# Kernel tuning notes

Hardware: AMD Instinct MI355X
Metric: run time of the kernel (lower is better)

The kernel has to match this reference:

```python
import jax, jax.numpy as jnp
import numpy as np

# Static problem sizes
B, C, T, H, W = 2, 256, 16, 64, 64
N = 128                      # number of ROIs
OT, OH, OW = 2, 7, 7         # output_size (t, h, w)
SS, TS = 1.0, 1.0            # spatial_scale, temporal_scale
T_EXT_MAX, S_EXT_MAX = 16, 32  # max ROI extents (by construction of rois)
# adaptive_max_pool bin length is bounded by ceil(L/O)+1
KT = (T_EXT_MAX + OT - 1) // OT + 1   # 9
KS = (S_EXT_MAX + OH - 1) // OH + 1   # 6


def setup_inputs() -> dict:
    key = jax.random.key(0)
    features = jax.random.normal(key, (B, C, T, H, W), dtype=jnp.float32)
    rng = np.random.default_rng(0)
    bidx = rng.integers(0, B, N)
    te = rng.integers(4, T_EXT_MAX + 1, N)
    t1 = rng.integers(0, T - te + 1)
    t2 = t1 + te - 1
    he = rng.integers(8, S_EXT_MAX + 1, N)
    y1 = rng.integers(0, H - he + 1)
    y2 = y1 + he - 1
    we = rng.integers(8, S_EXT_MAX + 1, N)
    x1 = rng.integers(0, W - we + 1)
    x2 = x1 + we - 1
    # layout: (batch_idx, t1, x1, y1, t2, x2, y2)
    rois = np.stack([bidx, t1, x1, y1, t2, x2, y2], axis=1).astype(np.float32)
    return {"features": features, "rois": jnp.asarray(rois)}


def _bin_idx(start, length, O, K):
    """Adaptive-pool bin indices for one dim. Returns abs indices [O,K] and validity mask."""
    o = jnp.arange(O)
    s = (o * length) // O                      # floor(o*L/O)
    e = ((o + 1) * length + O - 1) // O        # ceil((o+1)*L/O)
    idx = s[:, None] + jnp.arange(K)[None, :]  # [O, K]
    valid = idx < e[:, None]
    return start + jnp.minimum(idx, length - 1), valid


def _pool_one(roi, features):
    b = roi[0].astype(jnp.int32)
    # source scales coords cols [1,2,3,4] by spatial_scale and [0,5] by temporal_scale
    scale = jnp.array([TS, SS, SS, SS, SS, TS], dtype=roi.dtype)
    c = jnp.floor(roi[1:7] * scale).astype(jnp.int32)
    t1, x1, y1, t2, x2, y2 = c[0], c[1], c[2], c[3], c[4], c[5]
    feat = features[b]  # [C, T, H, W]
    neg = -jnp.inf
    # W dimension
    wi, wv = _bin_idx(x1, x2 - x1 + 1, OW, KS)
    x = feat[:, :, :, wi]                                    # [C,T,H,OW,KS]
    x = jnp.where(wv, x, neg).max(axis=-1)                   # [C,T,H,OW]
    # H dimension
    hi, hv = _bin_idx(y1, y2 - y1 + 1, OH, KS)
    x = jnp.take(x, hi.reshape(-1), axis=2).reshape(C, T, OH, KS, OW)
    x = jnp.where(hv[None, None, :, :, None], x, neg).max(axis=3)  # [C,T,OH,OW]
    # T dimension
    ti, tv = _bin_idx(t1, t2 - t1 + 1, OT, KT)
    x = jnp.take(x, ti.reshape(-1), axis=1).reshape(C, OT, KT, OH, OW)
    return jnp.where(tv[None, :, :, None, None], x, neg).max(axis=2)  # [C,OT,OH,OW]


def reference(features, rois):
    # sequential map over ROIs keeps peak memory bounded (each ROI pool is fully vectorized)
    return jax.lax.map(lambda r: _pool_one(r, features), rois)  # [N,C,OT,OH,OW]
```

## Files before the change

kernel.cpp:

```cpp
#include <hip/hip_runtime.h>
#include <hip/hip_fp16.h>
#include <math.h>

#define BB 2
#define CC 256
#define TT 16
#define HH 64
#define WW 64
#define NN 128
#define OT 2
#define OH 7
#define OW 7
#define PP (TT * HH * WW)
#define BIN (OT * OH * OW)
#define CU2 (CC / 2)
#define NQ (NN * OH * OW)
#define GRIDP (NQ / 2)

typedef _Float16 hf2 __attribute__((ext_vector_type(2)));

__global__ __launch_bounds__(256) void transpose_f16_kernel(
    const float* __restrict__ in, unsigned int* __restrict__ outt )
{
    __shared__ float tile[64][65];
    int pb = blockIdx.x & 1023;
    int cb = (blockIdx.x >> 10) & 3;
    int b  = blockIdx.x >> 12;

    int tx = threadIdx.x & 63;
    int wv = threadIdx.x >> 6;
    const float* src = in + ((size_t)b * CC + cb * 64) * PP + pb * 64;
    #pragma unroll
    for (int r = 0; r < 16; ++r) {
        int c = wv + r * 4;
        tile[tx][c] = src[(size_t)c * PP + tx];
    }
    __syncthreads();

    int cp   = threadIdx.x & 31;
    int prow = threadIdx.x >> 5;
    size_t base = ((size_t)b * PP + (size_t)pb * 64) * CC + cb * 64;
    #pragma unroll
    for (int r = 0; r < 8; ++r) {
        int p = prow + r * 8;
        __half h0 = __float2half(tile[p][2 * cp]);
        __half h1 = __float2half(tile[p][2 * cp + 1]);
        unsigned int u = (unsigned int)__half_as_ushort(h0)
                       | ((unsigned int)__half_as_ushort(h1) << 16);
        outt[(base + (size_t)p * CC) / 2 + cp] = u;
    }
}

template<int NX, int D>
__device__ __forceinline__ void pool_loop(
    const unsigned int* __restrict__ p, int niter, int ny,
    int ystep, int tstep, hf2& m0, hf2& m1, hf2& m2, hf2& m3)
{
    uint4 v[D][NX];
    int iy = 0;

#define PLOAD(d)                                            \
    _Pragma("unroll")                                       \
    for (int j = 0; j < NX; ++j)                            \
        v[d][j] = *(const uint4*)(p + j * CU2);

#define PADV()                                              \
    do { if (++iy == ny) { iy = 0; p += tstep; } else p += ystep; } while (0)

#define PCONS(d)                                            \
    _Pragma("unroll")                                       \
    for (int j = 0; j < NX; ++j) {                          \
        m0 = __builtin_elementwise_max(m0, __builtin_bit_cast(hf2, v[d][j].x)); \
        m1 = __builtin_elementwise_max(m1, __builtin_bit_cast(hf2, v[d][j].y)); \
        m2 = __builtin_elementwise_max(m2, __builtin_bit_cast(hf2, v[d][j].z)); \
        m3 = __builtin_elementwise_max(m3, __builtin_bit_cast(hf2, v[d][j].w)); \
    }

    if (niter > D) {
        #pragma unroll
        for (int d = 0; d < D; ++d) { PLOAD(d); PADV(); }
        int M = (niter - D) / D;
        int r = (niter - D) % D;
        for (int s = 0; s < M; ++s) {
            #pragma unroll
            for (int d = 0; d < D; ++d) { PCONS(d); PLOAD(d); PADV(); }
        }
        #pragma unroll
        for (int d = 0; d < D - 1; ++d)
            if (d < r) { PCONS(d); PLOAD(d); PADV(); }
        #pragma unroll
        for (int d = 0; d < D; ++d) PCONS(d);
    } else {
        for (int i = 0; i < niter; ++i) { PLOAD(0); PADV(); PCONS(0); }
    }
#undef PLOAD
#undef PADV
#undef PCONS
}

__global__ __launch_bounds__(256) void roipool3d_f16_kernel(
    const unsigned int* __restrict__ featt,
    const float* __restrict__ rois,
    float* __restrict__ out)
{
    __shared__ unsigned int comb[2][64][4];

    int wg  = blockIdx.x;
    int swz = (wg & 7) * (GRIDP / 8) + (wg >> 3);
    int wave  = threadIdx.x >> 6;
    int qslot = wave >> 1;
    int tc    = wave & 1;
    int lane = threadIdx.x & 63;
    int half = lane >> 5;
    int cl   = lane & 31;
    int q    = swz * 2 + qslot;
    int rem  = q % (OH * OW);
    int n    = q / (OH * OW);
    int oh   = rem / OW;
    int ow   = rem % OW;

    const float* r = rois + n * 7;
    int b  = (int)r[0];
    int t1 = (int)r[1];
    int x1 = (int)r[2];
    int y1 = (int)r[3];
    int t2 = (int)r[4];
    int x2 = (int)r[5];
    int y2 = (int)r[6];
    int lt = t2 - t1 + 1, lh = y2 - y1 + 1, lw = x2 - x1 + 1;

    int nt_full = (lt + 1) >> 1;
    int ntc0 = (nt_full + 1) >> 1;
    int nt_c = tc ? (nt_full - ntc0) : ntc0;
    int t0 = t1 + (half ? (lt >> 1) : 0) + (tc ? ntc0 : 0);

    int hs = (oh * lh) / OH, he = ((oh + 1) * lh + OH - 1) / OH;
    int ws = (ow * lw) / OW, we = ((ow + 1) * lw + OW - 1) / OW;
    int ny = he - hs;
    int nx = we - ws;
    int niter = nt_c * ny;

    const unsigned int* p = featt
        + (size_t)((size_t)b * PP + (size_t)((t0 * HH + (y1 + hs)) * WW + (x1 + ws))) * CU2
        + cl * 4;

    const int ystep = WW * CU2;
    const int tstep = (HH - (ny - 1)) * WW * CU2;

    hf2 m0; m0[0] = (_Float16)(-65504.0f); m0[1] = m0[0];
    hf2 m1 = m0, m2 = m0, m3 = m0;

    switch (nx) {
        case 2:  pool_loop<2, 6>(p, niter, ny, ystep, tstep, m0, m1, m2, m3); break;
        case 3:  pool_loop<3, 4>(p, niter, ny, ystep, tstep, m0, m1, m2, m3); break;
        case 4:  pool_loop<4, 3>(p, niter, ny, ystep, tstep, m0, m1, m2, m3); break;
        case 5:  pool_loop<5, 2>(p, niter, ny, ystep, tstep, m0, m1, m2, m3); break;
        default: pool_loop<6, 2>(p, niter, ny, ystep, tstep, m0, m1, m2, m3); break;
    }

    if (tc) {
        comb[qslot][lane][0] = __builtin_bit_cast(unsigned int, m0);
        comb[qslot][lane][1] = __builtin_bit_cast(unsigned int, m1);
        comb[qslot][lane][2] = __builtin_bit_cast(unsigned int, m2);
        comb[qslot][lane][3] = __builtin_bit_cast(unsigned int, m3);
    }
    __syncthreads();
    if (!tc) {
        m0 = __builtin_elementwise_max(m0, __builtin_bit_cast(hf2, comb[qslot][lane][0]));
        m1 = __builtin_elementwise_max(m1, __builtin_bit_cast(hf2, comb[qslot][lane][1]));
        m2 = __builtin_elementwise_max(m2, __builtin_bit_cast(hf2, comb[qslot][lane][2]));
        m3 = __builtin_elementwise_max(m3, __builtin_bit_cast(hf2, comb[qslot][lane][3]));

        int c0 = cl * 8;
        int bin = half * (OH * OW) + rem;
        size_t ob = (size_t)(n * CC + c0) * BIN + bin;
        out[ob]           = (float)m0[0];
        out[ob + BIN]     = (float)m0[1];
        out[ob + 2 * BIN] = (float)m1[0];
        out[ob + 3 * BIN] = (float)m1[1];
        out[ob + 4 * BIN] = (float)m2[0];
        out[ob + 5 * BIN] = (float)m2[1];
        out[ob + 6 * BIN] = (float)m3[0];
        out[ob + 7 * BIN] = (float)m3[1];
    }
}

#define NXCD 8
#define C_PER_XCD (CC / NXCD)
#define PLANE (NN * BIN)
#define BLOCKS_PER_C (PLANE / 256)
__global__ __launch_bounds__(256) void roipool3d_fb_kernel(
    const float* __restrict__ feat, const float* __restrict__ rois,
    float* __restrict__ out)
{
    int wg = blockIdx.x, xcd = wg % NXCD, i = wg / NXCD;
    int c = xcd * C_PER_XCD + i / BLOCKS_PER_C;
    int p = (i % BLOCKS_PER_C) * 256 + threadIdx.x;
    int n = p / BIN, rem = p % BIN;
    int ot = rem / (OH * OW), oh = (rem / OW) % OH, ow = rem % OW;
    const float* r = rois + n * 7;
    int b = (int)r[0], t1 = (int)r[1], x1 = (int)r[2], y1 = (int)r[3];
    int t2 = (int)r[4], x2 = (int)r[5], y2 = (int)r[6];
    int lt = t2 - t1 + 1, lh = y2 - y1 + 1, lw = x2 - x1 + 1;
    int ts = (ot * lt) / OT, te = ((ot + 1) * lt + OT - 1) / OT;
    int hs = (oh * lh) / OH, he = ((oh + 1) * lh + OH - 1) / OH;
    int ws = (ow * lw) / OW, we = ((ow + 1) * lw + OW - 1) / OW;
    const float* fbase = feat + ((size_t)b * CC + c) * PP;
    float m = -INFINITY;
    for (int t = t1 + ts; t < t1 + te; ++t)
        for (int y = y1 + hs; y < y1 + he; ++y)
            for (int x = x1 + ws; x < x1 + we; ++x)
                m = fmaxf(m, fbase[t * (HH * WW) + y * WW + x]);
    out[((size_t)n * CC + c) * BIN + rem] = m;
}

extern "C" void kernel_launch(void* const* d_in, const int* in_sizes, int n_in,
                              void* d_out, int out_size, void* d_ws, size_t ws_size,
                              hipStream_t stream) {
    const float* feat = (const float*)d_in[0];
    const float* rois = (const float*)d_in[1];
    float* out = (float*)d_out;

    size_t need = (size_t)BB * CC * PP * sizeof(unsigned short);
    if (ws_size >= need && d_ws) {
        unsigned int* featt = (unsigned int*)d_ws;
        transpose_f16_kernel<<<BB * 4 * 1024, 256, 0, stream>>>(feat, featt);
        roipool3d_f16_kernel<<<GRIDP, 256, 0, stream>>>(featt, rois, out);
    } else {
        roipool3d_fb_kernel<<<NXCD * C_PER_XCD * BLOCKS_PER_C, 256, 0, stream>>>(
            feat, rois, out);
    }
}
```

Before: 84.11 us.

## Sort ROIs by Morton key and stage channel-contiguous output before untransposing

Adds a single-block bitonic sort that orders ROIs by batch index and a Morton code of their center, so neighbouring workgroups pool spatially nearby regions and share cache lines in the transposed feature buffer. The pooling kernel now writes vectorized channel-contiguous float4 results into a staging buffer instead of eight scattered strided stores. A new untranspose kernel then rewrites the staging buffer into the required [N,C,OT,OH,OW] layout through shared memory. This adds two kernel launches and an extra pass over the output in exchange for better cache locality and coalesced writes.

After: 83.54 us, median of 2. Within noise of the previous version (-0.7%).

```diff
diff --git a/kernel.cpp b/kernel.cpp
--- a/kernel.cpp
+++ b/kernel.cpp
@@ -17,6 +17,12 @@
 #define NQ (NN * OH * OW)
 #define GRIDP (NQ / 2)
 
+#define FEATT_BYTES ((size_t)BB * CC * PP * 2)
+#define STAGE_OFF   FEATT_BYTES
+#define STAGE_BYTES ((size_t)NN * BIN * CC * 4)
+#define PERM_OFF    (STAGE_OFF + ((STAGE_BYTES + 255) & ~(size_t)255))
+#define WS_NEED     (PERM_OFF + NN * 4)
+
 typedef _Float16 hf2 __attribute__((ext_vector_type(2)));
 
 __global__ __launch_bounds__(256) void transpose_f16_kernel(
@@ -49,6 +55,42 @@
                        | ((unsigned int)__half_as_ushort(h1) << 16);
         outt[(base + (size_t)p * CC) / 2 + cp] = u;
     }
+}
+
+__global__ __launch_bounds__(128) void sort_rois_kernel(
+    const float* __restrict__ rois, int* __restrict__ perm)
+{
+    __shared__ unsigned int k[NN];
+    int t = threadIdx.x;
+    const float* r = rois + t * 7;
+    int b  = (int)r[0];
+    int t1 = (int)r[1], x1 = (int)r[2], y1 = (int)r[3];
+    int t2 = (int)r[4], x2 = (int)r[5], y2 = (int)r[6];
+    int tc = (t1 + t2) >> 1;
+    int yc = ((y1 + y2) >> 1) >> 2;
+    int xc = ((x1 + x2) >> 1) >> 2;
+    unsigned int m = 0;
+    #pragma unroll
+    for (int i = 0; i < 4; ++i) {
+        m |= (((unsigned)(tc >> i) & 1u) << (3 * i + 2));
+        m |= (((unsigned)(yc >> i) & 1u) << (3 * i + 1));
+        m |= (((unsigned)(xc >> i) & 1u) << (3 * i));
+    }
+    unsigned int key = ((unsigned)b << 12) | m;
+    k[t] = (key << 8) | (unsigned)t;
+    __syncthreads();
+    for (int kk = 2; kk <= NN; kk <<= 1) {
+        for (int j = kk >> 1; j > 0; j >>= 1) {
+            int ixj = t ^ j;
+            if (ixj > t) {
+                bool up = ((t & kk) == 0);
+                unsigned int a = k[t], c = k[ixj];
+                if ((a > c) == up) { k[t] = c; k[ixj] = a; }
+            }
+            __syncthreads();
+        }
+    }
+    perm[t] = (int)(k[t] & 0xFFu);
 }
 
 template<int NX, int D>
@@ -101,7 +143,8 @@
 __global__ __launch_bounds__(256) void roipool3d_f16_kernel(
     const unsigned int* __restrict__ featt,
     const float* __restrict__ rois,
-    float* __restrict__ out)
+    const int* __restrict__ perm,
+    float* __restrict__ stage)
 {
     __shared__ unsigned int comb[2][64][4];
 
@@ -115,7 +158,7 @@
     int cl   = lane & 31;
     int q    = swz * 2 + qslot;
     int rem  = q % (OH * OW);
-    int n    = q / (OH * OW);
+    int n    = perm[q / (OH * OW)];
     int oh   = rem / OW;
     int ow   = rem % OW;
 
@@ -173,15 +216,30 @@
 
         int c0 = cl * 8;
         int bin = half * (OH * OW) + rem;
-        size_t ob = (size_t)(n * CC + c0) * BIN + bin;
-        out[ob]           = (float)m0[0];
-        out[ob + BIN]     = (float)m0[1];
-        out[ob + 2 * BIN] = (float)m1[0];
-        out[ob + 3 * BIN] = (float)m1[1];
-        out[ob + 4 * BIN] = (float)m2[0];
-        out[ob + 5 * BIN] = (float)m2[1];
-        out[ob + 6 * BIN] = (float)m3[0];
-        out[ob + 7 * BIN] = (float)m3[1];
+        float4 s0 = { (float)m0[0], (float)m0[1], (float)m1[0], (float)m1[1] };
+        float4 s1 = { (float)m2[0], (float)m2[1], (float)m3[0], (float)m3[1] };
+        float* sp = stage + ((size_t)n * BIN + bin) * CC + c0;
+        *(float4*)sp       = s0;
+        *(float4*)(sp + 4) = s1;
+    }
+}
+
+__global__ __launch_bounds__(128) void untranspose_kernel(
+    const float* __restrict__ stage, float* __restrict__ out)
+{
+    __shared__ float t[32][99];
+    int n  = blockIdx.x >> 3;
+    int c0 = (blockIdx.x & 7) * 32;
+    const float* sp = stage + (size_t)n * BIN * CC + c0;
+    for (int k = threadIdx.x; k < BIN * 32; k += 128) {
+        int bin = k >> 5, c = k & 31;
+        t[c][bin] = sp[(size_t)bin * CC + c];
+    }
+    __syncthreads();
+    float* op = out + ((size_t)n * CC + c0) * BIN;
+    for (int c = 0; c < 32; ++c) {
+        if (threadIdx.x < BIN)
+            op[(size_t)c * BIN + threadIdx.x] = t[c][threadIdx.x];
     }
 }
 
@@ -221,11 +279,14 @@
     const float* rois = (const float*)d_in[1];
     float* out = (float*)d_out;
 
-    size_t need = (size_t)BB * CC * PP * sizeof(unsigned short);
-    if (ws_size >= need && d_ws) {
+    if (ws_size >= WS_NEED && d_ws) {
         unsigned int* featt = (unsigned int*)d_ws;
+        float* stage = (float*)((char*)d_ws + STAGE_OFF);
+        int*   perm  = (int*)((char*)d_ws + PERM_OFF);
+        sort_rois_kernel<<<1, 128, 0, stream>>>(rois, perm);
         transpose_f16_kernel<<<BB * 4 * 1024, 256, 0, stream>>>(feat, featt);
-        roipool3d_f16_kernel<<<GRIDP, 256, 0, stream>>>(featt, rois, out);
+        roipool3d_f16_kernel<<<GRIDP, 256, 0, stream>>>(featt, rois, perm, stage);
+        untranspose_kernel<<<NN * 8, 128, 0, stream>>>(stage, out);
     } else {
         roipool3d_fb_kernel<<<NXCD * C_PER_XCD * BLOCKS_PER_C, 256, 0, stream>>>(
             feat, rois, out);
```
